# Kernel tuning notes

Measured on AMD Instinct MI355X. Metric: run time of the kernel, lower is better.

The kernel has to match this reference:

```python
import jax, jax.numpy as jnp
import numpy as np

B = 4_194_304  # batch of affine transforms
NDIMS = 3      # 3D registration -> (3, 4) affine matrices


def setup_inputs() -> dict:
    key = jax.random.key(0)
    # Affine 'shift' transforms (delta over identity), shape (B, N, N+1)
    trf = jax.random.normal(key, (B, NDIMS, NDIMS + 1), dtype=jnp.float32) * 0.1
    return {"trf": trf}


def reference(trf) -> jnp.ndarray:
    # trf: (B, N, N+1) affine shift matrices
    n = trf.shape[-2]
    b = trf.shape[0]
    # Pad with a zero bottom row -> (B, N+1, N+1), then add identity
    zeros_row = jnp.zeros((b, 1, n + 1), dtype=trf.dtype)
    padded = jnp.concatenate([trf, zeros_row], axis=1) + jnp.eye(n + 1, dtype=trf.dtype)
    # Batched inversion of (N+1)x(N+1) homogeneous matrices, keep top N rows
    inv = jnp.linalg.inv(padded)
    return inv[:, :n, :]
```

## Files before the change

kernel.cpp:

```cpp
#include <hip/hip_runtime.h>
#include <hip/hip_bf16.h>


__global__ __launch_bounds__(256) void InvertAffine_kernel(
    const float4* __restrict__ in, float4* __restrict__ out, int n) {
    int idx = blockIdx.x * blockDim.x + threadIdx.x;
    int stride = gridDim.x * blockDim.x;
    for (int i = idx; i < n; i += stride) {
        float4 r0 = in[i * 3 + 0];
        float4 r1 = in[i * 3 + 1];
        float4 r2 = in[i * 3 + 2];

        float a00 = 1.0f + r0.x, a01 = r0.y,        a02 = r0.z,        t0 = r0.w;
        float a10 = r1.x,        a11 = 1.0f + r1.y, a12 = r1.z,        t1 = r1.w;
        float a20 = r2.x,        a21 = r2.y,        a22 = 1.0f + r2.z, t2 = r2.w;

        float c00 = a11 * a22 - a12 * a21;
        float c01 = a12 * a20 - a10 * a22;
        float c02 = a10 * a21 - a11 * a20;
        float det = a00 * c00 + a01 * c01 + a02 * c02;
        float rdet = 1.0f / det;

        float i00 = c00 * rdet;
        float i01 = (a02 * a21 - a01 * a22) * rdet;
        float i02 = (a01 * a12 - a02 * a11) * rdet;
        float i10 = c01 * rdet;
        float i11 = (a00 * a22 - a02 * a20) * rdet;
        float i12 = (a02 * a10 - a00 * a12) * rdet;
        float i20 = c02 * rdet;
        float i21 = (a01 * a20 - a00 * a21) * rdet;
        float i22 = (a00 * a11 - a01 * a10) * rdet;

        float o0 = -(i00 * t0 + i01 * t1 + i02 * t2);
        float o1 = -(i10 * t0 + i11 * t1 + i12 * t2);
        float o2 = -(i20 * t0 + i21 * t1 + i22 * t2);

        out[i * 3 + 0] = make_float4(i00, i01, i02, o0);
        out[i * 3 + 1] = make_float4(i10, i11, i12, o1);
        out[i * 3 + 2] = make_float4(i20, i21, i22, o2);
    }
}

extern "C" void kernel_launch(void* const* d_in, const int* in_sizes, int n_in,
                              void* d_out, int out_size, void* d_ws, size_t ws_size,
                              hipStream_t stream) {
    const float4* in = (const float4*)d_in[0];
    float4* out = (float4*)d_out;
    int n = in_sizes[0] / 12;

    const int block = 256;
    int blocks = (n + block - 1) / block;
    if (blocks > 2048) blocks = 2048;
    InvertAffine_kernel<<<blocks, block, 0, stream>>>(in, out, n);
}
```

Baseline: 339.2 us.

## Stage affine matrices through LDS for fully coalesced global loads and stores

Each block now handles a tile of 256 matrices. It loads the tile's 768 float4 values in unit-stride order into shared memory, computes each inverse from LDS, writes the results back into LDS, and then stores them to global memory with unit stride. This replaces the earlier per-thread stride-3 float4 accesses, which split each wave's loads and stores across three times the address range. In exchange it adds three block-wide barriers per tile and extra LDS traffic. With the grid still capped at 2048 blocks, each block works through tiles one after another, which limits how many memory requests are in flight.

```diff
diff --git a/kernel.cpp b/kernel.cpp
--- a/kernel.cpp
+++ b/kernel.cpp
@@ -2,42 +2,84 @@
 #include <hip/hip_bf16.h>
 
 
-__global__ __launch_bounds__(256) void InvertAffine_kernel(
+constexpr int BLOCK = 256;
+constexpr int MPB = 256;
+
+__global__ __launch_bounds__(BLOCK) void InvertAffine_kernel(
     const float4* __restrict__ in, float4* __restrict__ out, int n) {
-    int idx = blockIdx.x * blockDim.x + threadIdx.x;
-    int stride = gridDim.x * blockDim.x;
-    for (int i = idx; i < n; i += stride) {
-        float4 r0 = in[i * 3 + 0];
-        float4 r1 = in[i * 3 + 1];
-        float4 r2 = in[i * 3 + 2];
+    __shared__ float4 lds[MPB * 3];
+    const int t = threadIdx.x;
+    const int ntiles = (n + MPB - 1) / MPB;
 
-        float a00 = 1.0f + r0.x, a01 = r0.y,        a02 = r0.z,        t0 = r0.w;
-        float a10 = r1.x,        a11 = 1.0f + r1.y, a12 = r1.z,        t1 = r1.w;
-        float a20 = r2.x,        a21 = r2.y,        a22 = 1.0f + r2.z, t2 = r2.w;
+    for (int tile = blockIdx.x; tile < ntiles; tile += gridDim.x) {
+        const int mbase = tile * MPB;
+        const int f4base = mbase * 3;
+        const int nm = min(MPB, n - mbase);
+        const int nf4 = nm * 3;
 
-        float c00 = a11 * a22 - a12 * a21;
-        float c01 = a12 * a20 - a10 * a22;
-        float c02 = a10 * a21 - a11 * a20;
-        float det = a00 * c00 + a01 * c01 + a02 * c02;
-        float rdet = 1.0f / det;
+        float4 v[3];
+        #pragma unroll
+        for (int k = 0; k < 3; ++k) {
+            int idx = t + k * BLOCK;
+            if (idx < nf4) v[k] = in[f4base + idx];
+        }
+        #pragma unroll
+        for (int k = 0; k < 3; ++k) {
+            int idx = t + k * BLOCK;
+            if (idx < nf4) lds[idx] = v[k];
+        }
+        __syncthreads();
 
-        float i00 = c00 * rdet;
-        float i01 = (a02 * a21 - a01 * a22) * rdet;
-        float i02 = (a01 * a12 - a02 * a11) * rdet;
-        float i10 = c01 * rdet;
-        float i11 = (a00 * a22 - a02 * a20) * rdet;
-        float i12 = (a02 * a10 - a00 * a12) * rdet;
-        float i20 = c02 * rdet;
-        float i21 = (a01 * a20 - a00 * a21) * rdet;
-        float i22 = (a00 * a11 - a01 * a10) * rdet;
+        float4 q0, q1, q2;
+        const bool act = (t < nm);
+        if (act) {
+            float4 r0 = lds[t * 3 + 0];
+            float4 r1 = lds[t * 3 + 1];
+            float4 r2 = lds[t * 3 + 2];
 
-        float o0 = -(i00 * t0 + i01 * t1 + i02 * t2);
-        float o1 = -(i10 * t0 + i11 * t1 + i12 * t2);
-        float o2 = -(i20 * t0 + i21 * t1 + i22 * t2);
+            float a00 = 1.0f + r0.x, a01 = r0.y,        a02 = r0.z,        t0 = r0.w;
+            float a10 = r1.x,        a11 = 1.0f + r1.y, a12 = r1.z,        t1 = r1.w;
+            float a20 = r2.x,        a21 = r2.y,        a22 = 1.0f + r2.z, t2 = r2.w;
 
-        out[i * 3 + 0] = make_float4(i00, i01, i02, o0);
-        out[i * 3 + 1] = make_float4(i10, i11, i12, o1);
-        out[i * 3 + 2] = make_float4(i20, i21, i22, o2);
+            float c00 = a11 * a22 - a12 * a21;
+            float c01 = a12 * a20 - a10 * a22;
+            float c02 = a10 * a21 - a11 * a20;
+            float det = a00 * c00 + a01 * c01 + a02 * c02;
+            float rdet = 1.0f / det;
+
+            float i00 = c00 * rdet;
+            float i01 = (a02 * a21 - a01 * a22) * rdet;
+            float i02 = (a01 * a12 - a02 * a11) * rdet;
+            float i10 = c01 * rdet;
+            float i11 = (a00 * a22 - a02 * a20) * rdet;
+            float i12 = (a02 * a10 - a00 * a12) * rdet;
+            float i20 = c02 * rdet;
+            float i21 = (a01 * a20 - a00 * a21) * rdet;
+            float i22 = (a00 * a11 - a01 * a10) * rdet;
+
+            float o0 = -(i00 * t0 + i01 * t1 + i02 * t2);
+            float o1 = -(i10 * t0 + i11 * t1 + i12 * t2);
+            float o2 = -(i20 * t0 + i21 * t1 + i22 * t2);
+
+            q0 = make_float4(i00, i01, i02, o0);
+            q1 = make_float4(i10, i11, i12, o1);
+            q2 = make_float4(i20, i21, i22, o2);
+        }
+        __syncthreads();
+
+        if (act) {
+            lds[t * 3 + 0] = q0;
+            lds[t * 3 + 1] = q1;
+            lds[t * 3 + 2] = q2;
+        }
+        __syncthreads();
+
+        #pragma unroll
+        for (int k = 0; k < 3; ++k) {
+            int idx = t + k * BLOCK;
+            if (idx < nf4) out[f4base + idx] = lds[idx];
+        }
+        __syncthreads();
     }
 }
 
@@ -48,8 +90,7 @@
     float4* out = (float4*)d_out;
     int n = in_sizes[0] / 12;
 
-    const int block = 256;
-    int blocks = (n + block - 1) / block;
-    if (blocks > 2048) blocks = 2048;
-    InvertAffine_kernel<<<blocks, block, 0, stream>>>(in, out, n);
+    int ntiles = (n + MPB - 1) / MPB;
+    int blocks = ntiles < 2048 ? ntiles : 2048;
+    InvertAffine_kernel<<<blocks, BLOCK, 0, stream>>>(in, out, n);
 }
```

Measured after the change: 365.6 us. +7.8%, slower.
